# Optimization experiments

Hardware: AMD Instinct MI355X
Metric: run time of the kernel (lower is better)

## Reference

```python
import jax, jax.numpy as jnp
import numpy as np

N_NODES = 10000
N_EDGES = 160000
ATOMIC_DIM = 16          # C: multiplicity of 0e input irreps
L_VALUES = [0, 1, 2]
EDGE_DIM = 16            # number of bessel basis functions
HIDDEN_DIM = 16          # H: multiplicity of each output irrep
RADIUS_CUTOFF = 6.0
DEGREE_NORM = 16.0
SILU_GAIN = 1.679177     # e3nn normalize2mom gain for silu
WEIGHT_NUMEL = len(L_VALUES) * ATOMIC_DIM * HIDDEN_DIM  # 768


def bessel_basis(dist, num_basis, cutoff):
    # e3nn soft_one_hot_linspace, basis='bessel', start=0, cutoff=True
    x = dist[:, None]                                   # [E,1]
    n = jnp.arange(1, num_basis + 1, dtype=dist.dtype) * jnp.pi
    x_safe = jnp.where(x > 0, x, 1.0)
    out = jnp.sqrt(2.0 / cutoff) * jnp.sin(n * x / cutoff) / x_safe
    out = out * ((x < cutoff) & (x > 0))
    return out * jnp.sqrt(float(num_basis))             # EdgeEmbedding scaling


def spherical_harmonics(u):
    # e3nn real spherical harmonics l=0,1,2, 'component' convention, then
    # 'integral' normalization (divide by sqrt(4*pi)). u: unit vectors [E,3].
    x, y, z = u[:, 0], u[:, 1], u[:, 2]
    s3, s5, s15 = jnp.sqrt(3.0), jnp.sqrt(5.0), jnp.sqrt(15.0)
    y0 = jnp.ones_like(x)[:, None]
    y1 = jnp.stack([s3 * x, s3 * y, s3 * z], axis=-1)
    y2 = jnp.stack([
        s15 * x * z,
        s15 * x * y,
        s5 * (y * y - 0.5 * (x * x + z * z)),
        s15 * y * z,
        0.5 * s15 * (z * z - x * x),
    ], axis=-1)
    Y = jnp.concatenate([y0, y1, y2], axis=-1)          # [E, 9]
    return Y / jnp.sqrt(4.0 * jnp.pi)


def setup_inputs() -> dict:
    key = jax.random.key(0)
    k1, k2, k3, k4, k5 = jax.random.split(key, 5)
    atomic_features = jax.random.normal(k1, (N_NODES, ATOMIC_DIM), dtype=jnp.float32)
    coords = jax.random.normal(k2, (N_NODES, 3), dtype=jnp.float32) * 3.0
    edge_index = jax.random.randint(k3, (2, N_EDGES), 0, N_NODES, dtype=jnp.int64)
    W1 = jax.random.normal(k4, (EDGE_DIM, HIDDEN_DIM), dtype=jnp.float32)
    W2 = jax.random.normal(k5, (HIDDEN_DIM, WEIGHT_NUMEL), dtype=jnp.float32)
    return {"atomic_features": atomic_features, "coords": coords,
            "edge_index": edge_index, "W1": W1, "W2": W2}


def reference(atomic_features, coords, edge_index, W1, W2):
    src, dst = edge_index[0], edge_index[1]
    rel = coords[src] - coords[dst]                     # [E,3]
    dist = jnp.linalg.norm(rel, axis=-1)                # [E]
    # 1. spherical harmonic projection of normalized edge vectors
    u = rel / jnp.maximum(dist, 1e-12)[:, None]
    Y = spherical_harmonics(u)                          # [E,9]
    # 2. radial bessel basis
    eb = bessel_basis(dist, EDGE_DIM, RADIUS_CUTOFF)    # [E,edge_dim]
    # 3. FC net (e3nn FullyConnectedNet: /sqrt(fan_in), normalized silu)
    h = SILU_GAIN * jax.nn.silu(eb @ W1 / jnp.sqrt(float(EDGE_DIM)))
    edge_z = h @ W2 / jnp.sqrt(float(HIDDEN_DIM))       # [E, weight_numel]
    # 4. fully-connected tensor product Cx0e x (1x0e+1x1o+1x2e) -> Hx(...)
    E = edge_z.shape[0]
    w = edge_z.reshape(E, len(L_VALUES), ATOMIC_DIM, HIDDEN_DIM)
    xs = atomic_features[src]                           # [E,C]
    inv_sqrt_c = 1.0 / jnp.sqrt(float(ATOMIC_DIM))      # e3nn path normalization
    outs, off = [], 0
    for i, l in enumerate(L_VALUES):
        d = 2 * l + 1
        Yl = Y[:, off:off + d]                          # [E,d]
        m = jnp.einsum('ec,em,ech->ehm', xs, Yl, w[:, i]) * inv_sqrt_c
        outs.append(m.reshape(E, HIDDEN_DIM * d))
        off += d
    messages = jnp.concatenate(outs, axis=-1)           # [E, H*9]
    # 5. scatter-aggregate by destination node, degree normalization
    hidden = jax.ops.segment_sum(messages, dst, num_segments=N_NODES)
    return hidden / DEGREE_NORM
```

## Files before the change

### kernel.cpp

```cpp
#include <hip/hip_runtime.h>
#include <hip/hip_bf16.h>
#include <math.h>


typedef __attribute__((ext_vector_type(8))) short short8;
typedef __attribute__((ext_vector_type(4))) float f32x4;
typedef __attribute__((ext_vector_type(4))) unsigned short u16x4;

#define DSTRIDE 72

static __device__ __forceinline__ unsigned short f2bf(float f) {
  __hip_bfloat16 h = __float2bfloat16(f);
  return __builtin_bit_cast(unsigned short, h);
}
static __device__ __forceinline__ float bf2f(unsigned short s) {
  unsigned u = ((unsigned)s) << 16;
  return __builtin_bit_cast(float, u);
}

__global__ __launch_bounds__(256)
void prep_kernel(const float* __restrict__ W2, unsigned short* __restrict__ w2f,
                 int* __restrict__ head, int N) {
  int gid = blockIdx.x * 256 + threadIdx.x;
  if (gid < N) head[gid] = -1;
  if (gid < 24 * 64) {
    int fi = gid >> 6, lane = gid & 63;
    int s = fi / 3, t = fi - 3 * s;
    int h = lane & 15, kq = lane >> 4;
    short8 pack;
    #pragma unroll
    for (int j = 0; j < 8; ++j) {
      int kg = s * 32 + kq * 8 + j;
      int kk = kg >> 4, c = kg & 15;
      pack[j] = (short)f2bf(W2[kk * 768 + t * 256 + c * 16 + h]);
    }
    *(short8*)&w2f[(size_t)gid * 8] = pack;
  }
}

__global__ __launch_bounds__(256, 4)
void interact_kernel(const float* __restrict__ xfeat,
                     const float* __restrict__ coords,
                     const int* __restrict__ eidx,
                     const float* __restrict__ W1g,
                     const unsigned short* __restrict__ w2f,
                     unsigned short* __restrict__ data,
                     int* __restrict__ head,
                     int* __restrict__ next,
                     int E)
{
  __shared__ __align__(16) float W1s[256];
  __shared__ float hsS[64 * 20];
  __shared__ __align__(16) unsigned short xsS[64 * 24];
  __shared__ int eS[64];
  __shared__ int wsum[4];

  const int tid  = threadIdx.x;
  const int lane = tid & 63, wid = tid >> 6;
  const int q    = lane & 3;
  const int el   = wid * 16 + (lane >> 2);
  W1s[tid] = W1g[tid];

  const int e = blockIdx.x * 64 + el;
  bool act = false;
  int src = 0, dst = 0;
  float rx = 0.f, ry = 0.f, rz = 0.f, d2 = 0.f;
  if (e < E) {
    src = eidx[e]; dst = eidx[E + e];
    rx = coords[3*src]   - coords[3*dst];
    ry = coords[3*src+1] - coords[3*dst+1];
    rz = coords[3*src+2] - coords[3*dst+2];
    d2 = rx*rx + ry*ry + rz*rz;
    act = (d2 > 0.0f) && (d2 < 36.0f);
  }
  const float4 xq = *(const float4*)&xfeat[src*16 + q*4];

  unsigned long long bm = __ballot(act);
  unsigned long long emask = bm & 0x1111111111111111ull;
  int pfx = __popcll(emask & ((1ull << (4 * (lane >> 2))) - 1ull));
  if (lane == 0) wsum[wid] = __popcll(emask);
  __syncthreads();
  int base = 0;
  #pragma unroll
  for (int w = 0; w < 4; ++w) base += (w < wid) ? wsum[w] : 0;
  const int total = wsum[0] + wsum[1] + wsum[2] + wsum[3];
  const int cpos = base + pfx;

  if (act) {
    float dd  = sqrtf(d2);
    float inv = 1.0f / dd;
    if (q == 0) {
      float x = rx*inv, y = ry*inv, z = rz*inv;
      const float A1 = 0.48860251190291992f;
      const float A2 = 1.09254843059207907f;
      const float A3 = 0.63078313050504001f;
      unsigned short* dr = data + (size_t)e * DSTRIDE;
      short8 ys;
      ys[0] = (short)f2bf(A1*x);   ys[1] = (short)f2bf(A1*y);  ys[2] = (short)f2bf(A1*z);
      ys[3] = (short)f2bf(A2*x*z); ys[4] = (short)f2bf(A2*x*y);
      ys[5] = (short)f2bf(A3*(y*y - 0.5f*(x*x + z*z)));
      ys[6] = (short)f2bf(A2*y*z); ys[7] = (short)f2bf(0.5f*A2*(z*z - x*x));
      *(short8*)&dr[64] = ys;
      next[e] = atomicExch(&head[dst], e);
      eS[cpos] = e;
    }
    float theta = 0.52359877559829887f * dd;
    float s1 = __sinf(theta), c1 = __cosf(theta);
    float snm = 0.0f, sn = s1;
    float4 hb = make_float4(0.f, 0.f, 0.f, 0.f);
    #pragma unroll
    for (int k = 0; k < 16; ++k) {
      const float4 w = *((const float4*)&W1s[k*16 + q*4]);
      hb.x = fmaf(sn, w.x, hb.x);
      hb.y = fmaf(sn, w.y, hb.y);
      hb.z = fmaf(sn, w.z, hb.z);
      hb.w = fmaf(sn, w.w, hb.w);
      float sp = 2.0f*c1*sn - snm;
      snm = sn; sn = sp;
    }
    const float scale1 = 2.30940107675850305f * inv * 0.25f;
    float4 hv;
    {
      float b[4] = {hb.x, hb.y, hb.z, hb.w};
      float* op = (float*)&hv;
      #pragma unroll
      for (int r = 0; r < 4; ++r) {
        float p = b[r] * scale1;
        op[r] = 1.679177f * p / (1.0f + __expf(-p));
      }
    }
    *(float4*)&hsS[cpos * 20 + q * 4] = hv;
    u16x4 xp;
    xp[0] = f2bf(xq.x); xp[1] = f2bf(xq.y); xp[2] = f2bf(xq.z); xp[3] = f2bf(xq.w);
    *(u16x4*)&xsS[cpos * 24 + q * 4] = xp;
  }
  const int padded = (total + 15) & ~15;
  if (el >= total && el < padded) {
    *(float4*)&hsS[el * 20 + q * 4] = make_float4(0.f, 0.f, 0.f, 0.f);
    u16x4 z; z[0] = 0; z[1] = 0; z[2] = 0; z[3] = 0;
    *(u16x4*)&xsS[el * 24 + q * 4] = z;
  }
  __syncthreads();

  const int ngroups = padded >> 4;
  const int ma = lane & 15, kq = lane >> 4;
  const int c0 = (kq & 1) * 8;
  for (int g = wid; g < ngroups; g += 4) {
    const int cidx = g*16 + ma;
    const float* hrow = &hsS[cidx * 20];
    const unsigned short* xrow = &xsS[cidx * 24];
    float xsf[8];
    #pragma unroll
    for (int j = 0; j < 8; ++j) xsf[j] = bf2f(xrow[c0 + j]);

    f32x4 acc0 = {0,0,0,0}, acc1 = {0,0,0,0}, acc2 = {0,0,0,0};
    #pragma unroll
    for (int s = 0; s < 8; ++s) {
      const float hk = hrow[2*s + (kq >> 1)];
      short8 a;
      #pragma unroll
      for (int j = 0; j < 8; ++j) a[j] = (short)f2bf(hk * xsf[j]);
      const short8 b0 = *(const short8*)&w2f[(size_t)((s*3 + 0)*64 + lane) * 8];
      const short8 b1 = *(const short8*)&w2f[(size_t)((s*3 + 1)*64 + lane) * 8];
      const short8 b2 = *(const short8*)&w2f[(size_t)((s*3 + 2)*64 + lane) * 8];
      acc0 = __builtin_amdgcn_mfma_f32_16x16x32_bf16(a, b0, acc0, 0, 0, 0);
      acc1 = __builtin_amdgcn_mfma_f32_16x16x32_bf16(a, b1, acc1, 0, 0, 0);
      acc2 = __builtin_amdgcn_mfma_f32_16x16x32_bf16(a, b2, acc2, 0, 0, 0);
    }
    const float sc = 0.00390625f;
    #pragma unroll
    for (int r = 0; r < 4; ++r) {
      const int cr = g*16 + kq*4 + r;
      if (cr < total) {
        unsigned short* dr = data + (size_t)eS[cr] * DSTRIDE;
        u16x4 vv;
        vv[0] = f2bf(acc0[r] * sc);
        vv[1] = f2bf(acc1[r] * sc);
        vv[2] = f2bf(acc2[r] * sc);
        vv[3] = 0;
        *(u16x4*)&dr[ma * 4] = vv;
      }
    }
  }
}

__global__ __launch_bounds__(256)
void gather_kernel(const unsigned short* __restrict__ data,
                   const int* __restrict__ head,
                   const int* __restrict__ next,
                   float* __restrict__ out, int N)
{
  int gid = blockIdx.x * 256 + threadIdx.x;
  int node = gid >> 4, h = gid & 15;
  if (node >= N) return;

  float a0 = 0.f;
  float a10 = 0.f, a11 = 0.f, a12 = 0.f;
  float a20 = 0.f, a21 = 0.f, a22 = 0.f, a23 = 0.f, a24 = 0.f;

  int p = head[node];
  while (p >= 0) {
    const unsigned short* dr = data + (size_t)p * DSTRIDE;
    int pn = next[p];
    u16x4 vv = *(const u16x4*)&dr[h * 4];
    short8 yv = *(const short8*)&dr[64];
    float v0 = bf2f(vv[0]), v1 = bf2f(vv[1]), v2 = bf2f(vv[2]);
    a0  += v0;
    a10 = fmaf(v1, bf2f((unsigned short)yv[0]), a10);
    a11 = fmaf(v1, bf2f((unsigned short)yv[1]), a11);
    a12 = fmaf(v1, bf2f((unsigned short)yv[2]), a12);
    a20 = fmaf(v2, bf2f((unsigned short)yv[3]), a20);
    a21 = fmaf(v2, bf2f((unsigned short)yv[4]), a21);
    a22 = fmaf(v2, bf2f((unsigned short)yv[5]), a22);
    a23 = fmaf(v2, bf2f((unsigned short)yv[6]), a23);
    a24 = fmaf(v2, bf2f((unsigned short)yv[7]), a24);
    p = pn;
  }

  float* o = out + (size_t)node * 144;
  o[h] = a0 * 0.28209479177387814f;
  o[16 + h*3 + 0] = a10;
  o[16 + h*3 + 1] = a11;
  o[16 + h*3 + 2] = a12;
  o[64 + h*5 + 0] = a20;
  o[64 + h*5 + 1] = a21;
  o[64 + h*5 + 2] = a22;
  o[64 + h*5 + 3] = a23;
  o[64 + h*5 + 4] = a24;
}

extern "C" void kernel_launch(void* const* d_in, const int* in_sizes, int n_in,
                              void* d_out, int out_size, void* d_ws, size_t ws_size,
                              hipStream_t stream) {
  const float* xfeat  = (const float*)d_in[0];
  const float* coords = (const float*)d_in[1];
  const int*   eidx   = (const int*)d_in[2];
  const float* W1     = (const float*)d_in[3];
  const float* W2     = (const float*)d_in[4];
  float* out = (float*)d_out;

  const int E = in_sizes[2] / 2;
  const int N = out_size / 144;

  char* ws = (char*)d_ws;
  size_t off_head = (size_t)E * DSTRIDE * sizeof(unsigned short);
  size_t off_next = off_head + (size_t)((N + 3) & ~3) * sizeof(int);
  size_t off_w2f  = off_next + (size_t)E * sizeof(int);
  unsigned short* data = (unsigned short*)ws;
  int* head = (int*)(ws + off_head);
  int* next = (int*)(ws + off_next);
  unsigned short* w2f = (unsigned short*)(ws + off_w2f);

  int pblk = (N + 255) / 256;
  if (pblk < 6) pblk = 6;
  prep_kernel<<<pblk, 256, 0, stream>>>(W2, w2f, head, N);
  interact_kernel<<<(E + 63) / 64, 256, 0, stream>>>(xfeat, coords, eidx, W1,
                                                     w2f, data, head, next, E);
  gather_kernel<<<(N * 16 + 255) / 256, 256, 0, stream>>>(data, head, next, out, N);
}
```

Baseline: 41.58 us.

## Use single-wave blocks of 16 edges and drop active-edge compaction

The interact kernel now launches one 64-thread wavefront per block handling 16 edges, instead of 256-thread blocks handling 64 edges with ballot/prefix compaction of active edges. Each wave runs exactly one MFMA group over its 16 edges, inactive edges are zero-padded, and output rows are written directly by edge index using the ballot mask. This removes the cross-wave prefix sum, the shared-memory index table and the loop over variable group counts. In exchange, MFMA work is spent on out-of-cutoff edges, and each small block reloads W1 into shared memory and pays its own launch and barrier cost.

```diff
diff --git a/kernel.cpp b/kernel.cpp
--- a/kernel.cpp
+++ b/kernel.cpp
@@ -38,7 +38,7 @@
   }
 }
 
-__global__ __launch_bounds__(256, 4)
+__global__ __launch_bounds__(64, 4)
 void interact_kernel(const float* __restrict__ xfeat,
                      const float* __restrict__ coords,
                      const int* __restrict__ eidx,
@@ -50,18 +50,15 @@
                      int E)
 {
   __shared__ __align__(16) float W1s[256];
-  __shared__ float hsS[64 * 20];
-  __shared__ __align__(16) unsigned short xsS[64 * 24];
-  __shared__ int eS[64];
-  __shared__ int wsum[4];
-
-  const int tid  = threadIdx.x;
-  const int lane = tid & 63, wid = tid >> 6;
-  const int q    = lane & 3;
-  const int el   = wid * 16 + (lane >> 2);
-  W1s[tid] = W1g[tid];
-
-  const int e = blockIdx.x * 64 + el;
+  __shared__ float hsS[16 * 20];
+  __shared__ __align__(16) unsigned short xsS[16 * 24];
+
+  const int tid = threadIdx.x;
+  const int q   = tid & 3;
+  const int el  = tid >> 2;
+  *(float4*)&W1s[tid * 4] = *(const float4*)&W1g[tid * 4];
+
+  const int e = blockIdx.x * 16 + el;
   bool act = false;
   int src = 0, dst = 0;
   float rx = 0.f, ry = 0.f, rz = 0.f, d2 = 0.f;
@@ -75,16 +72,7 @@
   }
   const float4 xq = *(const float4*)&xfeat[src*16 + q*4];
 
-  unsigned long long bm = __ballot(act);
-  unsigned long long emask = bm & 0x1111111111111111ull;
-  int pfx = __popcll(emask & ((1ull << (4 * (lane >> 2))) - 1ull));
-  if (lane == 0) wsum[wid] = __popcll(emask);
-  __syncthreads();
-  int base = 0;
-  #pragma unroll
-  for (int w = 0; w < 4; ++w) base += (w < wid) ? wsum[w] : 0;
-  const int total = wsum[0] + wsum[1] + wsum[2] + wsum[3];
-  const int cpos = base + pfx;
+  const unsigned long long bm = __ballot(act);
 
   if (act) {
     float dd  = sqrtf(d2);
@@ -102,7 +90,6 @@
       ys[6] = (short)f2bf(A2*y*z); ys[7] = (short)f2bf(0.5f*A2*(z*z - x*x));
       *(short8*)&dr[64] = ys;
       next[e] = atomicExch(&head[dst], e);
-      eS[cpos] = e;
     }
     float theta = 0.52359877559829887f * dd;
     float s1 = __sinf(theta), c1 = __cosf(theta);
@@ -129,57 +116,51 @@
         op[r] = 1.679177f * p / (1.0f + __expf(-p));
       }
     }
-    *(float4*)&hsS[cpos * 20 + q * 4] = hv;
+    *(float4*)&hsS[el * 20 + q * 4] = hv;
     u16x4 xp;
     xp[0] = f2bf(xq.x); xp[1] = f2bf(xq.y); xp[2] = f2bf(xq.z); xp[3] = f2bf(xq.w);
-    *(u16x4*)&xsS[cpos * 24 + q * 4] = xp;
-  }
-  const int padded = (total + 15) & ~15;
-  if (el >= total && el < padded) {
+    *(u16x4*)&xsS[el * 24 + q * 4] = xp;
+  } else {
     *(float4*)&hsS[el * 20 + q * 4] = make_float4(0.f, 0.f, 0.f, 0.f);
     u16x4 z; z[0] = 0; z[1] = 0; z[2] = 0; z[3] = 0;
     *(u16x4*)&xsS[el * 24 + q * 4] = z;
   }
   __syncthreads();
 
-  const int ngroups = padded >> 4;
-  const int ma = lane & 15, kq = lane >> 4;
+  const int ma = tid & 15, kq = tid >> 4;
   const int c0 = (kq & 1) * 8;
-  for (int g = wid; g < ngroups; g += 4) {
-    const int cidx = g*16 + ma;
-    const float* hrow = &hsS[cidx * 20];
-    const unsigned short* xrow = &xsS[cidx * 24];
-    float xsf[8];
+  const float* hrow = &hsS[ma * 20];
+  const unsigned short* xrow = &xsS[ma * 24];
+  float xsf[8];
+  #pragma unroll
+  for (int j = 0; j < 8; ++j) xsf[j] = bf2f(xrow[c0 + j]);
+
+  f32x4 acc0 = {0,0,0,0}, acc1 = {0,0,0,0}, acc2 = {0,0,0,0};
+  #pragma unroll
+  for (int s = 0; s < 8; ++s) {
+    const float hk = hrow[2*s + (kq >> 1)];
+    short8 a;
     #pragma unroll
-    for (int j = 0; j < 8; ++j) xsf[j] = bf2f(xrow[c0 + j]);
-
-    f32x4 acc0 = {0,0,0,0}, acc1 = {0,0,0,0}, acc2 = {0,0,0,0};
-    #pragma unroll
-    for (int s = 0; s < 8; ++s) {
-      const float hk = hrow[2*s + (kq >> 1)];
-      short8 a;
-      #pragma unroll
-      for (int j = 0; j < 8; ++j) a[j] = (short)f2bf(hk * xsf[j]);
-      const short8 b0 = *(const short8*)&w2f[(size_t)((s*3 + 0)*64 + lane) * 8];
-      const short8 b1 = *(const short8*)&w2f[(size_t)((s*3 + 1)*64 + lane) * 8];
-      const short8 b2 = *(const short8*)&w2f[(size_t)((s*3 + 2)*64 + lane) * 8];
-      acc0 = __builtin_amdgcn_mfma_f32_16x16x32_bf16(a, b0, acc0, 0, 0, 0);
-      acc1 = __builtin_amdgcn_mfma_f32_16x16x32_bf16(a, b1, acc1, 0, 0, 0);
-      acc2 = __builtin_amdgcn_mfma_f32_16x16x32_bf16(a, b2, acc2, 0, 0, 0);
-    }
-    const float sc = 0.00390625f;
-    #pragma unroll
-    for (int r = 0; r < 4; ++r) {
-      const int cr = g*16 + kq*4 + r;
-      if (cr < total) {
-        unsigned short* dr = data + (size_t)eS[cr] * DSTRIDE;
-        u16x4 vv;
-        vv[0] = f2bf(acc0[r] * sc);
-        vv[1] = f2bf(acc1[r] * sc);
-        vv[2] = f2bf(acc2[r] * sc);
-        vv[3] = 0;
-        *(u16x4*)&dr[ma * 4] = vv;
-      }
+    for (int j = 0; j < 8; ++j) a[j] = (short)f2bf(hk * xsf[j]);
+    const short8 b0 = *(const short8*)&w2f[(size_t)((s*3 + 0)*64 + tid) * 8];
+    const short8 b1 = *(const short8*)&w2f[(size_t)((s*3 + 1)*64 + tid) * 8];
+    const short8 b2 = *(const short8*)&w2f[(size_t)((s*3 + 2)*64 + tid) * 8];
+    acc0 = __builtin_amdgcn_mfma_f32_16x16x32_bf16(a, b0, acc0, 0, 0, 0);
+    acc1 = __builtin_amdgcn_mfma_f32_16x16x32_bf16(a, b1, acc1, 0, 0, 0);
+    acc2 = __builtin_amdgcn_mfma_f32_16x16x32_bf16(a, b2, acc2, 0, 0, 0);
+  }
+  const float sc = 0.00390625f;
+  #pragma unroll
+  for (int r = 0; r < 4; ++r) {
+    const int er = kq*4 + r;
+    if ((bm >> (4*er)) & 1ull) {
+      unsigned short* dr = data + (size_t)(blockIdx.x*16 + er) * DSTRIDE;
+      u16x4 vv;
+      vv[0] = f2bf(acc0[r] * sc);
+      vv[1] = f2bf(acc1[r] * sc);
+      vv[2] = f2bf(acc2[r] * sc);
+      vv[3] = 0;
+      *(u16x4*)&dr[ma * 4] = vv;
     }
   }
 }
@@ -254,7 +235,7 @@
   int pblk = (N + 255) / 256;
   if (pblk < 6) pblk = 6;
   prep_kernel<<<pblk, 256, 0, stream>>>(W2, w2f, head, N);
-  interact_kernel<<<(E + 63) / 64, 256, 0, stream>>>(xfeat, coords, eidx, W1,
-                                                     w2f, data, head, next, E);
+  interact_kernel<<<(E + 15) / 16, 64, 0, stream>>>(xfeat, coords, eidx, W1,
+                                                    w2f, data, head, next, E);
   gather_kernel<<<(N * 16 + 255) / 256, 256, 0, stream>>>(data, head, next, out, N);
 }
```

New measurement: 37.81 us. -9.1%, faster.
